# Kernel tuning notes

Measured on AMD Instinct MI355X. Metric: run time of the kernel, lower is better.

The kernel has to match this reference:

```python
import jax, jax.numpy as jnp
import numpy as np

B, N, H, DH, E, D_IN = 2, 2048, 8, 32, 65536, 256
O = H * DH
SCALE = float(np.sqrt(DH))


def setup_inputs() -> dict:
    key = jax.random.key(0)
    ks = jax.random.split(key, 8)
    rng = np.random.default_rng(0)
    x = jax.random.normal(ks[0], (B, N, D_IN), jnp.float32)
    adj = jax.random.uniform(ks[1], (B, N, N), jnp.float32)
    # unique edges per graph so scatter-add matches torch advanced-index +=
    flat = np.stack([rng.choice(N * N, size=E, replace=False) for _ in range(B)])
    edge_index = jnp.asarray(np.stack([flat // N, flat % N], axis=1), jnp.int32)  # [B,2,E]
    edge_attr = jax.random.normal(ks[2], (B, E, H), jnp.float32)
    mask = jnp.ones((B, N), dtype=bool)
    qkv_w = jax.random.normal(ks[3], (D_IN, 3 * O), jnp.float32) / np.sqrt(D_IN)
    qkv_b = jnp.zeros((3 * O,), jnp.float32)
    e_w1 = jax.random.normal(ks[4], (H, H), jnp.float32) / np.sqrt(H)
    e_b1 = jnp.zeros((H,), jnp.float32)
    e_w2 = jax.random.normal(ks[5], (H, H), jnp.float32) / np.sqrt(H)
    e_b2 = jnp.zeros((H,), jnp.float32)
    shifts = jnp.asarray(np.linspace(0.1, 0.8, H), jnp.float32).reshape(1, H, 1, 1)
    widths = jnp.full((1, H, 1, 1), 0.5, jnp.float32)
    self_loop_W = jnp.asarray(1.0 / DH + rng.uniform(0, 1, H), jnp.float32).reshape(1, H, 1, 1)
    return dict(x=x, adj=adj, edge_attr=edge_attr, qkv_w=qkv_w, qkv_b=qkv_b,
                e_w1=e_w1, e_b1=e_b1, e_w2=e_w2, e_b2=e_b2,
                shifts=shifts, widths=widths, self_loop_W=self_loop_W,
                edge_index=edge_index, mask=mask)


def reference(x, adj, edge_attr, qkv_w, qkv_b, e_w1, e_b1, e_w2, e_b2,
              shifts, widths, self_loop_W, edge_index, mask):
    Bq, Nq = x.shape[0], x.shape[1]
    # qkv projection -> [3,B,H,N,DH]
    qkv = (x @ qkv_w + qkv_b).reshape(Bq, Nq, 3, H, DH)
    qkv = jnp.transpose(qkv, (2, 0, 3, 1, 4))
    Q, K, V = qkv[0], qkv[1], qkv[2]
    # edge FFN applied twice (eval mode: noise/dropout are identity)
    def ffn(e):
        return jax.nn.relu(e @ e_w1 + e_b1) @ e_w2 + e_b2
    ea = ffn(ffn(edge_attr))                      # [B,E,H]
    ea = jnp.transpose(ea, (0, 2, 1))             # [B,H,E]
    # scores + learned moire adjacency bias
    scores = jnp.einsum('bhqd,bhkd->bhqk', Q, K) / SCALE
    moire = jnp.exp(-((adj[:, None] - shifts) ** 2) / (2.0 * widths ** 2))  # gaussian focus
    moire = jnp.clip(moire, 1e-6, None)
    s = scores + jnp.log(moire)                   # [B,H,N,N]
    # scatter edge features into score matrix
    u = edge_index[:, 0, :]                        # [B,E]
    v = edge_index[:, 1, :]
    bi = jnp.arange(Bq)[:, None, None]
    hi = jnp.arange(H)[None, :, None]
    s = s.at[bi, hi, u[:, None, :], v[:, None, :]].add(ea)
    # self-loop diagonal bias (non-trainable)
    s = s + jnp.eye(Nq, dtype=s.dtype)[None, None] * self_loop_W
    # mask and softmax
    m2 = mask[:, None, :] & mask[:, :, None]       # [B,N,N]
    s = jnp.where(m2[:, None], s, jnp.asarray(-1e6, s.dtype))
    attn = jax.nn.softmax(s, axis=-1)
    out = jnp.einsum('bhqk,bhkd->bhqd', attn, V)
    return jnp.transpose(out, (0, 2, 1, 3)).reshape(Bq, Nq, O)
```

## Files before the change

kernel.cpp:

```cpp
#include <hip/hip_runtime.h>

#define B_ 2
#define N_ 2048
#define H_ 8
#define DH_ 32
#define E_ 65536
#define DIN_ 256
#define KT 256
#define NKT (N_ / KT)
#define ECAP 32
#define QSCALE 0.2550348872f
#define LOG2E 1.4426950408889634f
#define LOG2MIN -19.931568569324174f

typedef short bf16x8 __attribute__((ext_vector_type(8)));
typedef float floatx4 __attribute__((ext_vector_type(4)));

__device__ __forceinline__ unsigned short f2b(float f){
  union { float f; unsigned int u; } v; v.f = f;
  return (unsigned short)((v.u + 0x7fffu + ((v.u >> 16) & 1u)) >> 16);
}
__device__ __forceinline__ bf16x8 f8_to_bf(const float* p){
  float4 a = *(const float4*)p, b = *(const float4*)(p + 4);
  bf16x8 r;
  r[0] = (short)f2b(a.x); r[1] = (short)f2b(a.y); r[2] = (short)f2b(a.z); r[3] = (short)f2b(a.w);
  r[4] = (short)f2b(b.x); r[5] = (short)f2b(b.y); r[6] = (short)f2b(b.z); r[7] = (short)f2b(b.w);
  return r;
}
__device__ __forceinline__ unsigned int cvt_pk_bf16(float lo, float hi){
  unsigned int r;
  asm("v_cvt_pk_bf16_f32 %0, %1, %2" : "=v"(r) : "v"(lo), "v"(hi));
  return r;
}
__device__ __forceinline__ float fexp2(float x){
  float r;
  asm("v_exp_f32 %0, %1" : "=v"(r) : "v"(x));
  return r;
}

__global__ __launch_bounds__(256) void prep_kernel(
    const float* __restrict__ eattr,
    const float* __restrict__ w1, const float* __restrict__ b1,
    const float* __restrict__ w2, const float* __restrict__ b2,
    float* __restrict__ ea,
    const int* __restrict__ ei, int* __restrict__ cnt, unsigned int* __restrict__ pck,
    const float* __restrict__ w, unsigned short* __restrict__ wT)
{
  int bb = blockIdx.x, tid = threadIdx.x;
  if (bb < 512){
    __shared__ float W1[64], W2[64], Bv1[8], Bv2[8];
    if (tid < 64){ W1[tid] = w1[tid]; W2[tid] = w2[tid]; }
    if (tid < 8){ Bv1[tid] = b1[tid]; Bv2[tid] = b2[tid]; }
    __syncthreads();
    int gid = bb * 256 + tid;
    const float* ep = eattr + (size_t)gid * 8;
    float cur[8];
#pragma unroll
    for (int i = 0; i < 8; ++i) cur[i] = ep[i];
#pragma unroll
    for (int pass = 0; pass < 2; ++pass){
      float t[8];
#pragma unroll
      for (int j = 0; j < 8; ++j){
        float s = Bv1[j];
#pragma unroll
        for (int i = 0; i < 8; ++i) s += cur[i] * W1[i * 8 + j];
        t[j] = fmaxf(s, 0.f);
      }
#pragma unroll
      for (int j = 0; j < 8; ++j){
        float s = Bv2[j];
#pragma unroll
        for (int i = 0; i < 8; ++i) s += t[i] * W2[i * 8 + j];
        cur[j] = s;
      }
    }
    float* op = ea + (size_t)gid * 8;
#pragma unroll
    for (int j = 0; j < 8; ++j) op[j] = cur[j] * LOG2E;
  } else if (bb < 1024){
    int gid = (bb - 512) * 256 + tid;
    int b = gid >> 16, e = gid & (E_ - 1);
    int u = ei[(size_t)b * 2 * E_ + e];
    int v = ei[(size_t)b * 2 * E_ + E_ + e];
    int bucket = ((b << 11) + u) * 8 + (v >> 8);
    int slot = atomicAdd(&cnt[bucket], 1);
    if (slot < ECAP) pck[(size_t)bucket * ECAP + slot] = ((unsigned int)e << 11) | (unsigned int)v;
  } else {
    int k = bb - 1024;
    for (int c = tid; c < 768; c += 256)
      wT[(size_t)c * 256 + k] = f2b(w[(size_t)k * 768 + c]);
  }
}

__global__ __launch_bounds__(256) void qkv_kernel(
    const float* __restrict__ x, const unsigned short* __restrict__ wT,
    const float* __restrict__ bias,
    unsigned short* __restrict__ Qb, unsigned short* __restrict__ Kb, unsigned short* __restrict__ Vt)
{
  int tid = threadIdx.x;
  int wave = tid >> 6, lane = tid & 63, m = lane & 15, quad = lane >> 4;
  int rowbase = blockIdx.x * 16;
  int colbase = blockIdx.y * 64 + wave * 16;
  floatx4 acc = {0.f, 0.f, 0.f, 0.f};
#pragma unroll
  for (int kb = 0; kb < 8; ++kb){
    bf16x8 af = f8_to_bf(x + (size_t)(rowbase + m) * DIN_ + kb * 32 + quad * 8);
    bf16x8 bf = *(const bf16x8*)(wT + (size_t)(colbase + m) * DIN_ + kb * 32 + quad * 8);
    acc = __builtin_amdgcn_mfma_f32_16x16x32_bf16(af, bf, acc, 0, 0, 0);
  }
  int ccol = colbase + m;
  int which = ccol >> 8, hh = (ccol >> 5) & 7, dh = ccol & 31;
  float bv = bias[ccol];
  int row0 = rowbase + quad * 4;
  int bidx = row0 >> 11, n0 = row0 & (N_ - 1);
  size_t bh = (size_t)(bidx * H_ + hh);
  if (which == 0){
#pragma unroll
    for (int r = 0; r < 4; ++r)
      Qb[(bh * N_ + n0 + r) * DH_ + dh] = f2b((acc[r] + bv) * QSCALE);
  } else if (which == 1){
#pragma unroll
    for (int r = 0; r < 4; ++r)
      Kb[(bh * N_ + n0 + r) * DH_ + dh] = f2b(acc[r] + bv);
  } else {
    ushort4 st;
    st.x = f2b(acc[0] + bv); st.y = f2b(acc[1] + bv);
    st.z = f2b(acc[2] + bv); st.w = f2b(acc[3] + bv);
    *(ushort4*)(Vt + (bh * DH_ + dh) * N_ + n0) = st;
  }
}

__global__ __launch_bounds__(256) void attn_kernel(
    const unsigned short* __restrict__ Qb, const unsigned short* __restrict__ Kb,
    const unsigned short* __restrict__ Vt, const float* __restrict__ adj,
    const float* __restrict__ ea, const int* __restrict__ cnt, const unsigned int* __restrict__ pck,
    const float* __restrict__ shifts, const float* __restrict__ widths,
    const float* __restrict__ selfW, float* __restrict__ out)
{
  __shared__ float S[4][16][68];
  __shared__ float mfin[4][16], lfin[4][16];

  int bid = blockIdx.x;
  int qt = bid & 127, h = (bid >> 7) & 7, b = bid >> 10;
  int qbase = qt * 16;
  int tid = threadIdx.x, wave = tid >> 6, lane = tid & 63, m = lane & 15, quad = lane >> 4;
  float shift_h = shifts[h];
  float w_h = widths[h];
  float i2w_h = LOG2E / (2.f * w_h * w_h);
  float selfW_h = selfW[h] * LOG2E;
  size_t krow = (size_t)(b * H_ + h) * N_;
  size_t vrow = (size_t)(b * H_ + h) * DH_;
  bf16x8 qfrag = *(const bf16x8*)(Qb + (krow + qbase + m) * DH_ + quad * 8);
  float (*Sw)[68] = S[wave];
  int wcol = wave * 64;

  int rr = lane >> 2, sl0 = lane & 3;
  const int* cntp = cnt + ((size_t)(b * N_) + qbase + rr) * 8;
  const unsigned int* pckp = pck + ((size_t)((b * N_ + qbase + rr) * 8)) * ECAP;
  const float* eabase = ea + (size_t)b * E_ * H_ + h;
  const float* adjp = adj + ((size_t)b * N_ + qbase + m) * N_ + wcol + quad * 8;
  const unsigned short* vp0 = Vt + (vrow + m) * N_ + wcol + quad * 8;
  const unsigned short* vp1 = Vt + (vrow + 16 + m) * N_ + wcol + quad * 8;
  const unsigned short* kp  = Kb + (krow + wcol + m) * DH_ + quad * 8;

  floatx4 sh4 = {shift_h, shift_h, shift_h, shift_h};
  floatx4 ni4 = {-i2w_h, -i2w_h, -i2w_h, -i2w_h};
  floatx4 lm4 = {LOG2MIN, LOG2MIN, LOG2MIN, LOG2MIN};

  float mcur = -1e30f, lcur = 0.f;
  floatx4 oacc0 = {0.f, 0.f, 0.f, 0.f};
  floatx4 oacc1 = {0.f, 0.f, 0.f, 0.f};

  int nb_c = cntp[0]; nb_c = nb_c > ECAP ? ECAP : nb_c;
  unsigned int pk0 = pckp[sl0];
  unsigned int pk1 = pckp[sl0 + 4];
  int c0_c = (int)(pk0 & (N_ - 1)) - wcol;
  int c1_c = (int)(pk1 & (N_ - 1)) - wcol;
  bool g0_c = (sl0 < nb_c) && ((unsigned)c0_c < 64u);
  bool g1_c = (sl0 + 4 < nb_c) && ((unsigned)c1_c < 64u);
  float ea0_c = 0.f, ea1_c = 0.f;
  if (g0_c) ea0_c = eabase[(size_t)(pk0 >> 11) * H_];
  if (g1_c) ea1_c = eabase[(size_t)(pk1 >> 11) * H_];

#pragma unroll
  for (int kt = 0; kt < NKT; ++kt){
    int k0 = kt * KT;
    int nb_n = 0; unsigned int pk0_n = 0, pk1_n = 0;
    if (kt + 1 < NKT){
      nb_n  = cntp[kt + 1];
      pk0_n = pckp[(kt + 1) * ECAP + sl0];
      pk1_n = pckp[(kt + 1) * ECAP + sl0 + 4];
    }
    const float* ap = adjp + k0;
    floatx4 a00 = *(const floatx4*)(ap);
    floatx4 a01 = *(const floatx4*)(ap + 4);
    floatx4 a10 = *(const floatx4*)(ap + 32);
    floatx4 a11 = *(const floatx4*)(ap + 36);

#pragma unroll
    for (int s = 0; s < 4; ++s){
      bf16x8 kf = *(const bf16x8*)(kp + (size_t)(k0 + s * 16) * DH_);
      floatx4 acc = {0.f, 0.f, 0.f, 0.f};
      acc = __builtin_amdgcn_mfma_f32_16x16x32_bf16(qfrag, kf, acc, 0, 0, 0);
#pragma unroll
      for (int r = 0; r < 4; ++r)
        Sw[quad * 4 + r][s * 16 + m] = acc[r];
    }
    {
      int dw = qbase - k0 - wcol;
      if ((unsigned)dw < 64u && lane < 16)
        Sw[lane][dw + lane] += selfW_h;
    }
    if (g0_c) Sw[rr][c0_c] += ea0_c;
    if (g1_c) Sw[rr][c1_c] += ea1_c;
    if (nb_c > 8){
      for (int slot = sl0 + 8; slot < nb_c; slot += 4){
        unsigned int p = pckp[kt * ECAP + slot];
        int vv = (int)(p & (N_ - 1));
        int c = vv - k0 - wcol;
        if ((unsigned)c < 64u) Sw[rr][c] += eabase[(size_t)(p >> 11) * H_];
      }
    }
    int c0_n = 0, c1_n = 0; bool g0_n = false, g1_n = false;
    float ea0_n = 0.f, ea1_n = 0.f;
    if (kt + 1 < NKT){
      nb_n = nb_n > ECAP ? ECAP : nb_n;
      c0_n = (int)(pk0_n & (N_ - 1)) - (k0 + KT) - wcol;
      c1_n = (int)(pk1_n & (N_ - 1)) - (k0 + KT) - wcol;
      g0_n = (sl0 < nb_n) && ((unsigned)c0_n < 64u);
      g1_n = (sl0 + 4 < nb_n) && ((unsigned)c1_n < 64u);
      if (g0_n) ea0_n = eabase[(size_t)(pk0_n >> 11) * H_];
      if (g1_n) ea1_n = eabase[(size_t)(pk1_n >> 11) * H_];
    }
    bf16x8 vf00 = *(const bf16x8*)(vp0 + k0);
    bf16x8 vf01 = *(const bf16x8*)(vp1 + k0);
    bf16x8 vf10 = *(const bf16x8*)(vp0 + k0 + 32);
    bf16x8 vf11 = *(const bf16x8*)(vp1 + k0 + 32);

    const float* sp = &Sw[m][quad * 8];
    floatx4 s00 = *(const floatx4*)(sp);
    floatx4 s01 = *(const floatx4*)(sp + 4);
    floatx4 s10 = *(const floatx4*)(sp + 32);
    floatx4 s11 = *(const floatx4*)(sp + 36);
    floatx4 d;
    d = a00 - sh4; s00 += __builtin_elementwise_max(d * d * ni4, lm4);
    d = a01 - sh4; s01 += __builtin_elementwise_max(d * d * ni4, lm4);
    d = a10 - sh4; s10 += __builtin_elementwise_max(d * d * ni4, lm4);
    d = a11 - sh4; s11 += __builtin_elementwise_max(d * d * ni4, lm4);
    float lm = fmaxf(fmaxf(fmaxf(s00.x, s00.y), fmaxf(s00.z, s00.w)),
                     fmaxf(fmaxf(s01.x, s01.y), fmaxf(s01.z, s01.w)));
    lm = fmaxf(lm, fmaxf(fmaxf(fmaxf(s10.x, s10.y), fmaxf(s10.z, s10.w)),
                         fmaxf(fmaxf(s11.x, s11.y), fmaxf(s11.z, s11.w))));
    lm = fmaxf(lm, __shfl_xor(lm, 16));
    lm = fmaxf(lm, __shfl_xor(lm, 32));
    float mnew = fmaxf(mcur, lm);
    float al = fexp2(mcur - mnew);
    mcur = mnew;
    float al0 = __shfl(al, quad * 4 + 0);
    float al1 = __shfl(al, quad * 4 + 1);
    float al2 = __shfl(al, quad * 4 + 2);
    float al3 = __shfl(al, quad * 4 + 3);
    oacc0[0] *= al0; oacc0[1] *= al1; oacc0[2] *= al2; oacc0[3] *= al3;
    oacc1[0] *= al0; oacc1[1] *= al1; oacc1[2] *= al2; oacc1[3] *= al3;
    floatx4 m4 = {mcur, mcur, mcur, mcur};
    floatx4 e0v = s00 - m4, e1v = s01 - m4, e2v = s10 - m4, e3v = s11 - m4;
    float ps = 0.f, p0, p1;
    union { bf16x8 v; unsigned int u[4]; } P;
    p0 = fexp2(e0v.x); p1 = fexp2(e0v.y); ps += p0 + p1; P.u[0] = cvt_pk_bf16(p0, p1);
    p0 = fexp2(e0v.z); p1 = fexp2(e0v.w); ps += p0 + p1; P.u[1] = cvt_pk_bf16(p0, p1);
    p0 = fexp2(e1v.x); p1 = fexp2(e1v.y); ps += p0 + p1; P.u[2] = cvt_pk_bf16(p0, p1);
    p0 = fexp2(e1v.z); p1 = fexp2(e1v.w); ps += p0 + p1; P.u[3] = cvt_pk_bf16(p0, p1);
    oacc0 = __builtin_amdgcn_mfma_f32_16x16x32_bf16(P.v, vf00, oacc0, 0, 0, 0);
    oacc1 = __builtin_amdgcn_mfma_f32_16x16x32_bf16(P.v, vf01, oacc1, 0, 0, 0);
    p0 = fexp2(e2v.x); p1 = fexp2(e2v.y); ps += p0 + p1; P.u[0] = cvt_pk_bf16(p0, p1);
    p0 = fexp2(e2v.z); p1 = fexp2(e2v.w); ps += p0 + p1; P.u[1] = cvt_pk_bf16(p0, p1);
    p0 = fexp2(e3v.x); p1 = fexp2(e3v.y); ps += p0 + p1; P.u[2] = cvt_pk_bf16(p0, p1);
    p0 = fexp2(e3v.z); p1 = fexp2(e3v.w); ps += p0 + p1; P.u[3] = cvt_pk_bf16(p0, p1);
    oacc0 = __builtin_amdgcn_mfma_f32_16x16x32_bf16(P.v, vf10, oacc0, 0, 0, 0);
    oacc1 = __builtin_amdgcn_mfma_f32_16x16x32_bf16(P.v, vf11, oacc1, 0, 0, 0);
    ps += __shfl_xor(ps, 16);
    ps += __shfl_xor(ps, 32);
    lcur = lcur * al + ps;
    nb_c = nb_n; g0_c = g0_n; g1_c = g1_n;
    c0_c = c0_n; c1_c = c1_n; ea0_c = ea0_n; ea1_c = ea1_n;
  }

  if (quad == 0){ mfin[wave][m] = mcur; lfin[wave][m] = lcur; }
  float* Ow = &S[wave][0][0];
#pragma unroll
  for (int r = 0; r < 4; ++r){
    Ow[(quad * 4 + r) * 32 + m]      = oacc0[r];
    Ow[(quad * 4 + r) * 32 + 16 + m] = oacc1[r];
  }
  __syncthreads();
  const float* Sv = &S[0][0][0];
#pragma unroll
  for (int ii = 0; ii < 2; ++ii){
    int i = tid + ii * 256;
    int r = i >> 5, dcol = i & 31;
    float m0 = mfin[0][r], m1 = mfin[1][r], m2 = mfin[2][r], m3 = mfin[3][r];
    float mg = fmaxf(fmaxf(m0, m1), fmaxf(m2, m3));
    float w0 = fexp2(m0 - mg), w1 = fexp2(m1 - mg);
    float w2 = fexp2(m2 - mg), w3 = fexp2(m3 - mg);
    int o_idx = r * 32 + dcol;
    float o = Sv[o_idx] * w0 + Sv[1088 + o_idx] * w1
            + Sv[2176 + o_idx] * w2 + Sv[3264 + o_idx] * w3;
    float l = lfin[0][r] * w0 + lfin[1][r] * w1 + lfin[2][r] * w2 + lfin[3][r] * w3;
    out[((size_t)b * N_ + qbase + r) * (H_ * DH_) + h * DH_ + dcol] = o / l;
  }
}

extern "C" void kernel_launch(void* const* d_in, const int* in_sizes, int n_in,
                              void* d_out, int out_size, void* d_ws, size_t ws_size,
                              hipStream_t stream)
{
  const float* x      = (const float*)d_in[0];
  const float* adj    = (const float*)d_in[1];
  const float* eattr  = (const float*)d_in[2];
  const float* qkvw   = (const float*)d_in[3];
  const float* qkvb   = (const float*)d_in[4];
  const float* ew1    = (const float*)d_in[5];
  const float* eb1    = (const float*)d_in[6];
  const float* ew2    = (const float*)d_in[7];
  const float* eb2    = (const float*)d_in[8];
  const float* shifts = (const float*)d_in[9];
  const float* widths = (const float*)d_in[10];
  const float* selfW  = (const float*)d_in[11];
  const int*   ei     = (const int*)d_in[12];
  float* out = (float*)d_out;

  char* ws = (char*)d_ws;
  unsigned short* Qb  = (unsigned short*)(ws);
  unsigned short* Kb  = (unsigned short*)(ws + ((size_t)2 << 20));
  unsigned short* Vt  = (unsigned short*)(ws + ((size_t)4 << 20));
  unsigned short* wT  = (unsigned short*)(ws + ((size_t)6 << 20));
  float*          ea  = (float*)(ws + ((size_t)7 << 20));
  int*            cnt = (int*)(ws + ((size_t)11 << 20));
  unsigned int*  pck  = (unsigned int*)(ws + ((size_t)12 << 20));

  hipMemsetAsync(cnt, 0, (size_t)B_ * N_ * 8 * sizeof(int), stream);
  hipLaunchKernelGGL(prep_kernel, dim3(1280), dim3(256), 0, stream,
                     eattr, ew1, eb1, ew2, eb2, ea, ei, cnt, pck, qkvw, wT);
  hipLaunchKernelGGL(qkv_kernel, dim3(256, 12), dim3(256), 0, stream, x, wT, qkvb, Qb, Kb, Vt);
  hipLaunchKernelGGL(attn_kernel, dim3(B_ * H_ * (N_ / 16)), dim3(256), 0, stream,
                     Qb, Kb, Vt, adj, ea, cnt, pck, shifts, widths, selfW, out);
}
```

Before: 235.0 us.

## Give each wave a full key range per head and drop cross-wave softmax merge

Splits the attention work differently: each 128-thread block now covers two heads for one query tile, with one wave per head handling all 256 keys of each key tile, where before four waves each took a 64-key slice of a single head. This removes the shared-memory combine of per-wave max/sum/output and the block-level sync at the end, and lets each wave write its normalized output straight from registers. The block index is also remapped so blocks sharing the same query tile, and so the same adj rows, are grouped across XCDs for better L2 reuse. In exchange each wave holds a 16x256 score strip in LDS and many more live registers (sv[4][4]), and the key-tile loop is no longer unrolled, which may lower occupancy or lengthen the serial per-wave chain.

Result: faster. 222.2 us (-5.4%).

```diff
diff --git a/kernel.cpp b/kernel.cpp
--- a/kernel.cpp
+++ b/kernel.cpp
@@ -131,20 +131,23 @@
   }
 }
 
-__global__ __launch_bounds__(256) void attn_kernel(
+__global__ __launch_bounds__(128) void attn_kernel(
     const unsigned short* __restrict__ Qb, const unsigned short* __restrict__ Kb,
     const unsigned short* __restrict__ Vt, const float* __restrict__ adj,
     const float* __restrict__ ea, const int* __restrict__ cnt, const unsigned int* __restrict__ pck,
     const float* __restrict__ shifts, const float* __restrict__ widths,
     const float* __restrict__ selfW, float* __restrict__ out)
 {
-  __shared__ float S[4][16][68];
-  __shared__ float mfin[4][16], lfin[4][16];
+  __shared__ float S[2][16][260];
 
   int bid = blockIdx.x;
-  int qt = bid & 127, h = (bid >> 7) & 7, b = bid >> 10;
+  int xcd = bid & 7, t = bid >> 3;
+  int hp = t & 3;
+  int bqt = xcd * 32 + (t >> 2);
+  int b = bqt >> 7, qt = bqt & 127;
   int qbase = qt * 16;
   int tid = threadIdx.x, wave = tid >> 6, lane = tid & 63, m = lane & 15, quad = lane >> 4;
+  int h = hp * 2 + wave;
   float shift_h = shifts[h];
   float w_h = widths[h];
   float i2w_h = LOG2E / (2.f * w_h * w_h);
@@ -152,38 +155,36 @@
   size_t krow = (size_t)(b * H_ + h) * N_;
   size_t vrow = (size_t)(b * H_ + h) * DH_;
   bf16x8 qfrag = *(const bf16x8*)(Qb + (krow + qbase + m) * DH_ + quad * 8);
-  float (*Sw)[68] = S[wave];
-  int wcol = wave * 64;
+  float (*Sw)[260] = S[wave];
 
   int rr = lane >> 2, sl0 = lane & 3;
   const int* cntp = cnt + ((size_t)(b * N_) + qbase + rr) * 8;
   const unsigned int* pckp = pck + ((size_t)((b * N_ + qbase + rr) * 8)) * ECAP;
   const float* eabase = ea + (size_t)b * E_ * H_ + h;
-  const float* adjp = adj + ((size_t)b * N_ + qbase + m) * N_ + wcol + quad * 8;
-  const unsigned short* vp0 = Vt + (vrow + m) * N_ + wcol + quad * 8;
-  const unsigned short* vp1 = Vt + (vrow + 16 + m) * N_ + wcol + quad * 8;
-  const unsigned short* kp  = Kb + (krow + wcol + m) * DH_ + quad * 8;
+  const float* adjp = adj + ((size_t)b * N_ + qbase + m) * N_ + quad * 8;
+  const unsigned short* vp0 = Vt + (vrow + m) * N_ + quad * 8;
+  const unsigned short* vp1 = Vt + (vrow + 16 + m) * N_ + quad * 8;
+  const unsigned short* kp  = Kb + (krow + m) * DH_ + quad * 8;
 
   floatx4 sh4 = {shift_h, shift_h, shift_h, shift_h};
   floatx4 ni4 = {-i2w_h, -i2w_h, -i2w_h, -i2w_h};
   floatx4 lm4 = {LOG2MIN, LOG2MIN, LOG2MIN, LOG2MIN};
+  floatx4 z4  = {0.f, 0.f, 0.f, 0.f};
 
   float mcur = -1e30f, lcur = 0.f;
-  floatx4 oacc0 = {0.f, 0.f, 0.f, 0.f};
-  floatx4 oacc1 = {0.f, 0.f, 0.f, 0.f};
+  floatx4 oacc0 = z4, oacc1 = z4;
 
   int nb_c = cntp[0]; nb_c = nb_c > ECAP ? ECAP : nb_c;
   unsigned int pk0 = pckp[sl0];
   unsigned int pk1 = pckp[sl0 + 4];
-  int c0_c = (int)(pk0 & (N_ - 1)) - wcol;
-  int c1_c = (int)(pk1 & (N_ - 1)) - wcol;
-  bool g0_c = (sl0 < nb_c) && ((unsigned)c0_c < 64u);
-  bool g1_c = (sl0 + 4 < nb_c) && ((unsigned)c1_c < 64u);
+  int vv0_c = (int)(pk0 & (N_ - 1));
+  int vv1_c = (int)(pk1 & (N_ - 1));
+  bool g0_c = (sl0 < nb_c);
+  bool g1_c = (sl0 + 4 < nb_c);
   float ea0_c = 0.f, ea1_c = 0.f;
   if (g0_c) ea0_c = eabase[(size_t)(pk0 >> 11) * H_];
   if (g1_c) ea1_c = eabase[(size_t)(pk1 >> 11) * H_];
 
-#pragma unroll
   for (int kt = 0; kt < NKT; ++kt){
     int k0 = kt * KT;
     int nb_n = 0; unsigned int pk0_n = 0, pk1_n = 0;
@@ -192,66 +193,76 @@
       pk0_n = pckp[(kt + 1) * ECAP + sl0];
       pk1_n = pckp[(kt + 1) * ECAP + sl0 + 4];
     }
-    const float* ap = adjp + k0;
-    floatx4 a00 = *(const floatx4*)(ap);
-    floatx4 a01 = *(const floatx4*)(ap + 4);
-    floatx4 a10 = *(const floatx4*)(ap + 32);
-    floatx4 a11 = *(const floatx4*)(ap + 36);
-
-#pragma unroll
-    for (int s = 0; s < 4; ++s){
-      bf16x8 kf = *(const bf16x8*)(kp + (size_t)(k0 + s * 16) * DH_);
-      floatx4 acc = {0.f, 0.f, 0.f, 0.f};
-      acc = __builtin_amdgcn_mfma_f32_16x16x32_bf16(qfrag, kf, acc, 0, 0, 0);
-#pragma unroll
-      for (int r = 0; r < 4; ++r)
-        Sw[quad * 4 + r][s * 16 + m] = acc[r];
+#pragma unroll
+    for (int cb = 0; cb < 4; ++cb){
+      const unsigned short* kpb = kp + (size_t)(k0 + cb * 64) * DH_;
+#pragma unroll
+      for (int s = 0; s < 4; ++s){
+        bf16x8 kf = *(const bf16x8*)(kpb + (size_t)(s * 16) * DH_);
+        floatx4 acc = __builtin_amdgcn_mfma_f32_16x16x32_bf16(qfrag, kf, z4, 0, 0, 0);
+#pragma unroll
+        for (int r = 0; r < 4; ++r)
+          Sw[quad * 4 + r][cb * 64 + s * 16 + m] = acc[r];
+      }
     }
     {
-      int dw = qbase - k0 - wcol;
-      if ((unsigned)dw < 64u && lane < 16)
+      int dw = qbase - k0;
+      if ((unsigned)dw < 256u && lane < 16)
         Sw[lane][dw + lane] += selfW_h;
     }
-    if (g0_c) Sw[rr][c0_c] += ea0_c;
-    if (g1_c) Sw[rr][c1_c] += ea1_c;
+    if (g0_c) Sw[rr][vv0_c - k0] += ea0_c;
+    if (g1_c) Sw[rr][vv1_c - k0] += ea1_c;
     if (nb_c > 8){
       for (int slot = sl0 + 8; slot < nb_c; slot += 4){
         unsigned int p = pckp[kt * ECAP + slot];
-        int vv = (int)(p & (N_ - 1));
-        int c = vv - k0 - wcol;
-        if ((unsigned)c < 64u) Sw[rr][c] += eabase[(size_t)(p >> 11) * H_];
+        Sw[rr][(int)(p & (N_ - 1)) - k0] += eabase[(size_t)(p >> 11) * H_];
       }
     }
-    int c0_n = 0, c1_n = 0; bool g0_n = false, g1_n = false;
+    int vv0_n = 0, vv1_n = 0; bool g0_n = false, g1_n = false;
     float ea0_n = 0.f, ea1_n = 0.f;
     if (kt + 1 < NKT){
       nb_n = nb_n > ECAP ? ECAP : nb_n;
-      c0_n = (int)(pk0_n & (N_ - 1)) - (k0 + KT) - wcol;
-      c1_n = (int)(pk1_n & (N_ - 1)) - (k0 + KT) - wcol;
-      g0_n = (sl0 < nb_n) && ((unsigned)c0_n < 64u);
-      g1_n = (sl0 + 4 < nb_n) && ((unsigned)c1_n < 64u);
+      vv0_n = (int)(pk0_n & (N_ - 1));
+      vv1_n = (int)(pk1_n & (N_ - 1));
+      g0_n = (sl0 < nb_n);
+      g1_n = (sl0 + 4 < nb_n);
       if (g0_n) ea0_n = eabase[(size_t)(pk0_n >> 11) * H_];
       if (g1_n) ea1_n = eabase[(size_t)(pk1_n >> 11) * H_];
     }
-    bf16x8 vf00 = *(const bf16x8*)(vp0 + k0);
-    bf16x8 vf01 = *(const bf16x8*)(vp1 + k0);
-    bf16x8 vf10 = *(const bf16x8*)(vp0 + k0 + 32);
-    bf16x8 vf11 = *(const bf16x8*)(vp1 + k0 + 32);
-
-    const float* sp = &Sw[m][quad * 8];
-    floatx4 s00 = *(const floatx4*)(sp);
-    floatx4 s01 = *(const floatx4*)(sp + 4);
-    floatx4 s10 = *(const floatx4*)(sp + 32);
-    floatx4 s11 = *(const floatx4*)(sp + 36);
-    floatx4 d;
-    d = a00 - sh4; s00 += __builtin_elementwise_max(d * d * ni4, lm4);
-    d = a01 - sh4; s01 += __builtin_elementwise_max(d * d * ni4, lm4);
-    d = a10 - sh4; s10 += __builtin_elementwise_max(d * d * ni4, lm4);
-    d = a11 - sh4; s11 += __builtin_elementwise_max(d * d * ni4, lm4);
-    float lm = fmaxf(fmaxf(fmaxf(s00.x, s00.y), fmaxf(s00.z, s00.w)),
-                     fmaxf(fmaxf(s01.x, s01.y), fmaxf(s01.z, s01.w)));
-    lm = fmaxf(lm, fmaxf(fmaxf(fmaxf(s10.x, s10.y), fmaxf(s10.z, s10.w)),
-                         fmaxf(fmaxf(s11.x, s11.y), fmaxf(s11.z, s11.w))));
+    floatx4 sv[4][4];
+#pragma unroll
+    for (int cb = 0; cb < 4; ++cb){
+      const float* sp = &Sw[m][cb * 64 + quad * 8];
+      sv[cb][0] = *(const floatx4*)(sp);
+      sv[cb][1] = *(const floatx4*)(sp + 4);
+      sv[cb][2] = *(const floatx4*)(sp + 32);
+      sv[cb][3] = *(const floatx4*)(sp + 36);
+      const float* ap = adjp + k0 + cb * 64;
+      floatx4 a0 = *(const floatx4*)(ap);
+      floatx4 a1 = *(const floatx4*)(ap + 4);
+      floatx4 a2 = *(const floatx4*)(ap + 32);
+      floatx4 a3 = *(const floatx4*)(ap + 36);
+      floatx4 d;
+      d = a0 - sh4; sv[cb][0] += __builtin_elementwise_max(d * d * ni4, lm4);
+      d = a1 - sh4; sv[cb][1] += __builtin_elementwise_max(d * d * ni4, lm4);
+      d = a2 - sh4; sv[cb][2] += __builtin_elementwise_max(d * d * ni4, lm4);
+      d = a3 - sh4; sv[cb][3] += __builtin_elementwise_max(d * d * ni4, lm4);
+    }
+    floatx4 mx01 = __builtin_elementwise_max(
+        __builtin_elementwise_max(sv[0][0], sv[0][1]),
+        __builtin_elementwise_max(sv[0][2], sv[0][3]));
+    floatx4 mx23 = __builtin_elementwise_max(
+        __builtin_elementwise_max(sv[1][0], sv[1][1]),
+        __builtin_elementwise_max(sv[1][2], sv[1][3]));
+    floatx4 mx45 = __builtin_elementwise_max(
+        __builtin_elementwise_max(sv[2][0], sv[2][1]),
+        __builtin_elementwise_max(sv[2][2], sv[2][3]));
+    floatx4 mx67 = __builtin_elementwise_max(
+        __builtin_elementwise_max(sv[3][0], sv[3][1]),
+        __builtin_elementwise_max(sv[3][2], sv[3][3]));
+    floatx4 mxv = __builtin_elementwise_max(__builtin_elementwise_max(mx01, mx23),
+                                            __builtin_elementwise_max(mx45, mx67));
+    float lm = fmaxf(fmaxf(mxv.x, mxv.y), fmaxf(mxv.z, mxv.w));
     lm = fmaxf(lm, __shfl_xor(lm, 16));
     lm = fmaxf(lm, __shfl_xor(lm, 32));
     float mnew = fmaxf(mcur, lm);
@@ -264,51 +275,54 @@
     oacc0[0] *= al0; oacc0[1] *= al1; oacc0[2] *= al2; oacc0[3] *= al3;
     oacc1[0] *= al0; oacc1[1] *= al1; oacc1[2] *= al2; oacc1[3] *= al3;
     floatx4 m4 = {mcur, mcur, mcur, mcur};
-    floatx4 e0v = s00 - m4, e1v = s01 - m4, e2v = s10 - m4, e3v = s11 - m4;
-    float ps = 0.f, p0, p1;
-    union { bf16x8 v; unsigned int u[4]; } P;
-    p0 = fexp2(e0v.x); p1 = fexp2(e0v.y); ps += p0 + p1; P.u[0] = cvt_pk_bf16(p0, p1);
-    p0 = fexp2(e0v.z); p1 = fexp2(e0v.w); ps += p0 + p1; P.u[1] = cvt_pk_bf16(p0, p1);
-    p0 = fexp2(e1v.x); p1 = fexp2(e1v.y); ps += p0 + p1; P.u[2] = cvt_pk_bf16(p0, p1);
-    p0 = fexp2(e1v.z); p1 = fexp2(e1v.w); ps += p0 + p1; P.u[3] = cvt_pk_bf16(p0, p1);
-    oacc0 = __builtin_amdgcn_mfma_f32_16x16x32_bf16(P.v, vf00, oacc0, 0, 0, 0);
-    oacc1 = __builtin_amdgcn_mfma_f32_16x16x32_bf16(P.v, vf01, oacc1, 0, 0, 0);
-    p0 = fexp2(e2v.x); p1 = fexp2(e2v.y); ps += p0 + p1; P.u[0] = cvt_pk_bf16(p0, p1);
-    p0 = fexp2(e2v.z); p1 = fexp2(e2v.w); ps += p0 + p1; P.u[1] = cvt_pk_bf16(p0, p1);
-    p0 = fexp2(e3v.x); p1 = fexp2(e3v.y); ps += p0 + p1; P.u[2] = cvt_pk_bf16(p0, p1);
-    p0 = fexp2(e3v.z); p1 = fexp2(e3v.w); ps += p0 + p1; P.u[3] = cvt_pk_bf16(p0, p1);
-    oacc0 = __builtin_amdgcn_mfma_f32_16x16x32_bf16(P.v, vf10, oacc0, 0, 0, 0);
-    oacc1 = __builtin_amdgcn_mfma_f32_16x16x32_bf16(P.v, vf11, oacc1, 0, 0, 0);
+    floatx4 psv = z4;
+#pragma unroll
+    for (int cb = 0; cb < 4; ++cb){
+      const unsigned short* vA = vp0 + k0 + cb * 64;
+      const unsigned short* vB = vp1 + k0 + cb * 64;
+      bf16x8 vf00 = *(const bf16x8*)(vA);
+      bf16x8 vf01 = *(const bf16x8*)(vB);
+      bf16x8 vf10 = *(const bf16x8*)(vA + 32);
+      bf16x8 vf11 = *(const bf16x8*)(vB + 32);
+      floatx4 e0 = sv[cb][0] - m4, e1 = sv[cb][1] - m4;
+      floatx4 e2 = sv[cb][2] - m4, e3 = sv[cb][3] - m4;
+      floatx4 p0, p1, p2, p3;
+      p0.x = fexp2(e0.x); p0.y = fexp2(e0.y); p0.z = fexp2(e0.z); p0.w = fexp2(e0.w);
+      p1.x = fexp2(e1.x); p1.y = fexp2(e1.y); p1.z = fexp2(e1.z); p1.w = fexp2(e1.w);
+      p2.x = fexp2(e2.x); p2.y = fexp2(e2.y); p2.z = fexp2(e2.z); p2.w = fexp2(e2.w);
+      p3.x = fexp2(e3.x); p3.y = fexp2(e3.y); p3.z = fexp2(e3.z); p3.w = fexp2(e3.w);
+      psv += (p0 + p1) + (p2 + p3);
+      union { bf16x8 v; unsigned int u[4]; } PL, PH;
+      PL.u[0] = cvt_pk_bf16(p0.x, p0.y); PL.u[1] = cvt_pk_bf16(p0.z, p0.w);
+      PL.u[2] = cvt_pk_bf16(p1.x, p1.y); PL.u[3] = cvt_pk_bf16(p1.z, p1.w);
+      PH.u[0] = cvt_pk_bf16(p2.x, p2.y); PH.u[1] = cvt_pk_bf16(p2.z, p2.w);
+      PH.u[2] = cvt_pk_bf16(p3.x, p3.y); PH.u[3] = cvt_pk_bf16(p3.z, p3.w);
+      oacc0 = __builtin_amdgcn_mfma_f32_16x16x32_bf16(PL.v, vf00, oacc0, 0, 0, 0);
+      oacc1 = __builtin_amdgcn_mfma_f32_16x16x32_bf16(PL.v, vf01, oacc1, 0, 0, 0);
+      oacc0 = __builtin_amdgcn_mfma_f32_16x16x32_bf16(PH.v, vf10, oacc0, 0, 0, 0);
+      oacc1 = __builtin_amdgcn_mfma_f32_16x16x32_bf16(PH.v, vf11, oacc1, 0, 0, 0);
+    }
+    float ps = (psv.x + psv.y) + (psv.z + psv.w);
     ps += __shfl_xor(ps, 16);
     ps += __shfl_xor(ps, 32);
     lcur = lcur * al + ps;
     nb_c = nb_n; g0_c = g0_n; g1_c = g1_n;
-    c0_c = c0_n; c1_c = c1_n; ea0_c = ea0_n; ea1_c = ea1_n;
+    vv0_c = vv0_n; vv1_c = vv1_n; ea0_c = ea0_n; ea1_c = ea1_n;
   }
 
-  if (quad == 0){ mfin[wave][m] = mcur; lfin[wave][m] = lcur; }
-  float* Ow = &S[wave][0][0];
-#pragma unroll
-  for (int r = 0; r < 4; ++r){
-    Ow[(quad * 4 + r) * 32 + m]      = oacc0[r];
-    Ow[(quad * 4 + r) * 32 + 16 + m] = oacc1[r];
-  }
-  __syncthreads();
-  const float* Sv = &S[0][0][0];
-#pragma unroll
-  for (int ii = 0; ii < 2; ++ii){
-    int i = tid + ii * 256;
-    int r = i >> 5, dcol = i & 31;
-    float m0 = mfin[0][r], m1 = mfin[1][r], m2 = mfin[2][r], m3 = mfin[3][r];
-    float mg = fmaxf(fmaxf(m0, m1), fmaxf(m2, m3));
-    float w0 = fexp2(m0 - mg), w1 = fexp2(m1 - mg);
-    float w2 = fexp2(m2 - mg), w3 = fexp2(m3 - mg);
-    int o_idx = r * 32 + dcol;
-    float o = Sv[o_idx] * w0 + Sv[1088 + o_idx] * w1
-            + Sv[2176 + o_idx] * w2 + Sv[3264 + o_idx] * w3;
-    float l = lfin[0][r] * w0 + lfin[1][r] * w1 + lfin[2][r] * w2 + lfin[3][r] * w3;
-    out[((size_t)b * N_ + qbase + r) * (H_ * DH_) + h * DH_ + dcol] = o / l;
-  }
+  float linv0 = 1.f / __shfl(lcur, quad * 4 + 0);
+  float linv1 = 1.f / __shfl(lcur, quad * 4 + 1);
+  float linv2 = 1.f / __shfl(lcur, quad * 4 + 2);
+  float linv3 = 1.f / __shfl(lcur, quad * 4 + 3);
+  float* ob = out + ((size_t)b * N_ + qbase + quad * 4) * (H_ * DH_) + h * DH_;
+  ob[0 * H_ * DH_ + m]      = oacc0[0] * linv0;
+  ob[0 * H_ * DH_ + 16 + m] = oacc1[0] * linv0;
+  ob[1 * H_ * DH_ + m]      = oacc0[1] * linv1;
+  ob[1 * H_ * DH_ + 16 + m] = oacc1[1] * linv1;
+  ob[2 * H_ * DH_ + m]      = oacc0[2] * linv2;
+  ob[2 * H_ * DH_ + 16 + m] = oacc1[2] * linv2;
+  ob[3 * H_ * DH_ + m]      = oacc0[3] * linv3;
+  ob[3 * H_ * DH_ + 16 + m] = oacc1[3] * linv3;
 }
 
 extern "C" void kernel_launch(void* const* d_in, const int* in_sizes, int n_in,
@@ -343,6 +357,6 @@
   hipLaunchKernelGGL(prep_kernel, dim3(1280), dim3(256), 0, stream,
                      eattr, ew1, eb1, ew2, eb2, ea, ei, cnt, pck, qkvw, wT);
   hipLaunchKernelGGL(qkv_kernel, dim3(256, 12), dim3(256), 0, stream, x, wT, qkvb, Qb, Kb, Vt);
-  hipLaunchKernelGGL(attn_kernel, dim3(B_ * H_ * (N_ / 16)), dim3(256), 0, stream,
+  hipLaunchKernelGGL(attn_kernel, dim3(B_ * (H_ / 2) * (N_ / 16)), dim3(128), 0, stream,
                      Qb, Kb, Vt, adj, ea, cnt, pck, shifts, widths, selfW, out);
 }
```
